# Performance work log

Hardware: AMD Instinct MI355X
Metric: run time of the kernel (lower is better)

## Reference

```python
import jax, jax.numpy as jnp
import numpy as np

B, R, S = 4, 65536, 48  # batch, rays (256x256), depth_resolution


def setup_inputs() -> dict:
    key = jax.random.key(0)
    k1, k2, k3 = jax.random.split(key, 3)
    colors = jax.random.uniform(k1, (B, R, S, 3), dtype=jnp.float32)
    densities = jax.random.normal(k2, (B, R, S, 1), dtype=jnp.float32)
    # stratified depths in [-1, 1], monotone along sample axis (axis=-2)
    depths = jnp.sort(
        jax.random.uniform(k3, (B, R, S, 1), dtype=jnp.float32) * 2.0 - 1.0,
        axis=-2,
    )
    return {"colors": colors, "densities": densities, "depths": depths}


def reference(colors, densities, depths):
    # MipRayMarcher2.run_forward
    deltas = depths[:, :, 1:] - depths[:, :, :-1]                     # [B,R,S-1,1]
    colors_mid = (colors[:, :, :-1] + colors[:, :, 1:]) * 0.5         # [B,R,S-1,3]
    densities_mid = (densities[:, :, :-1] + densities[:, :, 1:]) * 0.5
    depths_mid = (depths[:, :, :-1] + depths[:, :, 1:]) * 0.5

    densities_mid = jax.nn.softplus(densities_mid - 1.0)
    density_delta = densities_mid * deltas
    alpha = 1.0 - jnp.exp(-density_delta)                             # [B,R,S-1,1]

    # exclusive cumulative transmittance along the sample axis
    alpha_shifted = jnp.concatenate(
        [jnp.ones_like(alpha[:, :, :1]), 1.0 - alpha + 1e-10], axis=-2
    )
    weights = alpha * jnp.cumprod(alpha_shifted, axis=-2)[:, :, :-1]  # [B,R,S-1,1]

    composite_rgb = jnp.sum(weights * colors_mid, axis=-2)            # [B,R,3]
    weight_total = jnp.sum(weights, axis=2)                           # [B,R,1]
    composite_depth = jnp.sum(weights * depths_mid, axis=-2) / weight_total
    composite_depth = jnp.nan_to_num(composite_depth, nan=jnp.inf)
    composite_depth = jnp.clip(composite_depth, jnp.min(depths), jnp.max(depths))

    composite_rgb = composite_rgb * 2.0 - 1.0
    return composite_rgb, composite_depth, weights
```

## Files before the change

kernel.cpp:

```cpp
#include <hip/hip_runtime.h>
#include <math.h>


#define S_SAMPLES 48
#define S_INTERVALS 47
#define WR 16
#define PAD 17
#define WAVES 2
#define BT (WAVES * 64)

#define A_OFF 0
#define B_OFF (S_SAMPLES * PAD)
#define WAVE_LDS (2 * S_SAMPLES * PAD)

__global__ __launch_bounds__(BT, 6) void raymarch_kernel(
    const float* __restrict__ colors,
    const float* __restrict__ densities,
    const float* __restrict__ depths,
    float* __restrict__ bmin,
    float* __restrict__ bmax,
    float* __restrict__ out_rgb,
    float* __restrict__ out_depth,
    float* __restrict__ out_w,
    int nRays) {
    __shared__ float smem[WAVES * WAVE_LDS];
    const int wid = threadIdx.x >> 6;
    const int lane = threadIdx.x & 63;
    float* Wb = smem + wid * WAVE_LDS;

    const int waveId = blockIdx.x * WAVES + wid;
    const size_t wray = (size_t)waveId * WR;

    {
        const float4* gdep = (const float4*)(depths + wray * S_SAMPLES);
        const float4* gden = (const float4*)(densities + wray * S_SAMPLES);
#pragma unroll
        for (int k = 0; k < 3; ++k) {
            int fidx = lane + k * 64;
            int g = fidx * 4;
            int ray = g / S_SAMPLES;
            int s = g - ray * S_SAMPLES;
            float4 vd = gdep[fidx];
            float4 vn = gden[fidx];
            Wb[A_OFF + (s + 0) * PAD + ray] = vd.x;
            Wb[A_OFF + (s + 1) * PAD + ray] = vd.y;
            Wb[A_OFF + (s + 2) * PAD + ray] = vd.z;
            Wb[A_OFF + (s + 3) * PAD + ray] = vd.w;
            Wb[B_OFF + (s + 0) * PAD + ray] = vn.x;
            Wb[B_OFF + (s + 1) * PAD + ray] = vn.y;
            Wb[B_OFF + (s + 2) * PAD + ray] = vn.z;
            Wb[B_OFF + (s + 3) * PAD + ray] = vn.w;
        }
    }

    const int r = lane >> 2;
    const int q = lane & 3;

    const float4* gcol4 = (const float4*)(colors + wray * (S_SAMPLES * 3));
    const int f0 = lane, f1 = lane + 64, f2 = lane + 128;
    const int rr0 = f0 / 12, i40 = f0 - rr0 * 12;
    const int rr1 = f1 / 12, i41 = f1 - rr1 * 12;
    const int rr2 = f2 / 12, i42 = f2 - rr2 * 12;
    float4 t0 = gcol4[rr0 * 36 + i40];
    float4 t1 = gcol4[rr1 * 36 + i41];
    float4 t2 = gcol4[rr2 * 36 + i42];

    asm volatile("s_waitcnt lgkmcnt(0)" ::: "memory");

    const int sBase = 12 * q;
    const float LOG2E = 1.4426950408889634f;
    float dPrev = Wb[A_OFF + sBase * PAD + r];
    float nPrev = Wb[B_OFF + sBase * PAD + r];
    const float firstDep = dPrev;

    float T = 1.f, aw = 0.f, ad = 0.f;
    float w0, w1, w2, w3, w4, w5, w6, w7, w8, w9, w10, w11;

#define MSTEP(J, W, HAS)                                               \
    do {                                                               \
        const int row = (HAS) ? (sBase + (J) + 1) : (sBase + 11);      \
        float dN = Wb[A_OFF + row * PAD + r];                          \
        float nN = Wb[B_OFF + row * PAD + r];                          \
        float delta = dN - dPrev;                                      \
        float xs = (0.5f * (nPrev + nN) - 1.f) * LOG2E;                \
        float sp2 = fmaxf(xs, 0.f) + log2f(1.f + exp2f(-fabsf(xs)));   \
        float alpha = (HAS) ? (1.f - exp2f(-delta * sp2)) : 0.f;       \
        W = alpha * T;                                                 \
        T *= (1.f - alpha + 1e-10f);                                   \
        aw += W;                                                       \
        ad = fmaf(W, 0.5f * (dPrev + dN), ad);                         \
        dPrev = dN;                                                    \
        nPrev = nN;                                                    \
    } while (0)

    MSTEP(0, w0, true);
    MSTEP(1, w1, true);
    MSTEP(2, w2, true);
    MSTEP(3, w3, true);
    MSTEP(4, w4, true);
    MSTEP(5, w5, true);
    MSTEP(6, w6, true);
    MSTEP(7, w7, true);
    MSTEP(8, w8, true);
    MSTEP(9, w9, true);
    MSTEP(10, w10, true);
    MSTEP(11, w11, (q < 3));
#undef MSTEP

    float P = T;
    float u1s = __shfl_up(P, 1);
    float pq = (q >= 1) ? P * u1s : P;
    float u2s = __shfl_up(pq, 2);
    float incl = (q >= 2) ? pq * u2s : pq;
    float u3s = __shfl_up(incl, 1);
    float Texc = (q >= 1) ? u3s : 1.f;

    Wb[A_OFF + (sBase + 0) * PAD + r] = w0 * Texc;
    Wb[A_OFF + (sBase + 1) * PAD + r] = w1 * Texc;
    Wb[A_OFF + (sBase + 2) * PAD + r] = w2 * Texc;
    Wb[A_OFF + (sBase + 3) * PAD + r] = w3 * Texc;
    Wb[A_OFF + (sBase + 4) * PAD + r] = w4 * Texc;
    Wb[A_OFF + (sBase + 5) * PAD + r] = w5 * Texc;
    Wb[A_OFF + (sBase + 6) * PAD + r] = w6 * Texc;
    Wb[A_OFF + (sBase + 7) * PAD + r] = w7 * Texc;
    Wb[A_OFF + (sBase + 8) * PAD + r] = w8 * Texc;
    Wb[A_OFF + (sBase + 9) * PAD + r] = w9 * Texc;
    Wb[A_OFF + (sBase + 10) * PAD + r] = w10 * Texc;
    if (q < 3) Wb[A_OFF + (sBase + 11) * PAD + r] = w11 * Texc;

    aw *= Texc;
    ad *= Texc;
#pragma unroll
    for (int off = 1; off <= 2; off <<= 1) {
        aw += __shfl_xor(aw, off);
        ad += __shfl_xor(ad, off);
    }
    if (q == 0) out_depth[wray + r] = ad / aw;

    float mnd = (q == 0) ? firstDep : INFINITY;
    float mxd = (q == 3) ? dPrev : -INFINITY;
#pragma unroll
    for (int off = 32; off; off >>= 1) {
        mnd = fminf(mnd, __shfl_xor(mnd, off));
        mxd = fmaxf(mxd, __shfl_xor(mxd, off));
    }
    if (lane == 0) {
        bmin[waveId] = mnd;
        bmax[waveId] = mxd;
    }

    asm volatile("s_waitcnt lgkmcnt(0)" ::: "memory");

    {
        float* gw = out_w + wray * S_INTERVALS;
#pragma unroll
        for (int k = 0; k < 12; ++k) {
            int g = lane + k * 64;
            if (g < WR * S_INTERVALS) {
                int ray = g / S_INTERVALS;
                int s = g - ray * S_INTERVALS;
                gw[g] = Wb[A_OFF + s * PAD + ray];
            }
        }
    }

    float a0 = 0.f, a1 = 0.f, a2 = 0.f;
#pragma unroll
    for (int c = 0; c < 3; ++c) {
        Wb[B_OFF + (i40 * 4 + 0) * PAD + rr0] = t0.x;
        Wb[B_OFF + (i40 * 4 + 1) * PAD + rr0] = t0.y;
        Wb[B_OFF + (i40 * 4 + 2) * PAD + rr0] = t0.z;
        Wb[B_OFF + (i40 * 4 + 3) * PAD + rr0] = t0.w;
        Wb[B_OFF + (i41 * 4 + 0) * PAD + rr1] = t1.x;
        Wb[B_OFF + (i41 * 4 + 1) * PAD + rr1] = t1.y;
        Wb[B_OFF + (i41 * 4 + 2) * PAD + rr1] = t1.z;
        Wb[B_OFF + (i41 * 4 + 3) * PAD + rr1] = t1.w;
        Wb[B_OFF + (i42 * 4 + 0) * PAD + rr2] = t2.x;
        Wb[B_OFF + (i42 * 4 + 1) * PAD + rr2] = t2.y;
        Wb[B_OFF + (i42 * 4 + 2) * PAD + rr2] = t2.z;
        Wb[B_OFF + (i42 * 4 + 3) * PAD + rr2] = t2.w;
        if (c < 2) {
            float4 n0 = gcol4[rr0 * 36 + (c + 1) * 12 + i40];
            float4 n1 = gcol4[rr1 * 36 + (c + 1) * 12 + i41];
            float4 n2 = gcol4[rr2 * 36 + (c + 1) * 12 + i42];
            asm volatile("s_waitcnt lgkmcnt(0)" ::: "memory");
#pragma unroll
            for (int i = 0; i < 4; ++i) {
                int sl = 4 * q + i;
                int s = c * 16 + sl;
                float wlo = (s >= 1) ? Wb[A_OFF + (s - 1) * PAD + r] : 0.f;
                float whi = (s <= 46) ? Wb[A_OFF + s * PAD + r] : 0.f;
                float v = 0.5f * (wlo + whi);
                a0 = fmaf(v, Wb[B_OFF + (3 * sl + 0) * PAD + r], a0);
                a1 = fmaf(v, Wb[B_OFF + (3 * sl + 1) * PAD + r], a1);
                a2 = fmaf(v, Wb[B_OFF + (3 * sl + 2) * PAD + r], a2);
            }
            t0 = n0;
            t1 = n1;
            t2 = n2;
        } else {
            asm volatile("s_waitcnt lgkmcnt(0)" ::: "memory");
#pragma unroll
            for (int i = 0; i < 4; ++i) {
                int sl = 4 * q + i;
                int s = c * 16 + sl;
                float wlo = (s >= 1) ? Wb[A_OFF + (s - 1) * PAD + r] : 0.f;
                float whi = (s <= 46) ? Wb[A_OFF + s * PAD + r] : 0.f;
                float v = 0.5f * (wlo + whi);
                a0 = fmaf(v, Wb[B_OFF + (3 * sl + 0) * PAD + r], a0);
                a1 = fmaf(v, Wb[B_OFF + (3 * sl + 1) * PAD + r], a1);
                a2 = fmaf(v, Wb[B_OFF + (3 * sl + 2) * PAD + r], a2);
            }
        }
    }

#pragma unroll
    for (int off = 1; off <= 2; off <<= 1) {
        a0 += __shfl_xor(a0, off);
        a1 += __shfl_xor(a1, off);
        a2 += __shfl_xor(a2, off);
    }
    if (q == 0) {
        size_t rb = (wray + r) * 3;
        out_rgb[rb + 0] = fmaf(a0, 2.f, -1.f);
        out_rgb[rb + 1] = fmaf(a1, 2.f, -1.f);
        out_rgb[rb + 2] = fmaf(a2, 2.f, -1.f);
    }
}

__global__ __launch_bounds__(1024) void reduce_minmax_kernel(
    const float* __restrict__ bmin, const float* __restrict__ bmax,
    float* __restrict__ g, int n) {
    float mn = INFINITY, mx = -INFINITY;
    for (int i = threadIdx.x; i < n; i += 1024) {
        mn = fminf(mn, bmin[i]);
        mx = fmaxf(mx, bmax[i]);
    }
#pragma unroll
    for (int off = 32; off; off >>= 1) {
        mn = fminf(mn, __shfl_xor(mn, off));
        mx = fmaxf(mx, __shfl_xor(mx, off));
    }
    __shared__ float smn[16], smx[16];
    const int wid = threadIdx.x >> 6;
    if ((threadIdx.x & 63) == 0) {
        smn[wid] = mn;
        smx[wid] = mx;
    }
    __syncthreads();
    if (threadIdx.x == 0) {
        float m = INFINITY, M = -INFINITY;
#pragma unroll
        for (int i = 0; i < 16; ++i) {
            m = fminf(m, smn[i]);
            M = fmaxf(M, smx[i]);
        }
        g[0] = m;
        g[1] = M;
    }
}

__global__ __launch_bounds__(256) void clamp_depth_kernel(
    float* __restrict__ out_depth, const float* __restrict__ g, int n) {
    int i = blockIdx.x * blockDim.x + threadIdx.x;
    if (i < n) {
        float gmin = g[0];
        float gmax = g[1];
        float d = out_depth[i];
        if (isnan(d)) d = INFINITY;
        d = fminf(fmaxf(d, gmin), gmax);
        out_depth[i] = d;
    }
}

extern "C" void kernel_launch(void* const* d_in, const int* in_sizes, int n_in,
                              void* d_out, int out_size, void* d_ws, size_t ws_size,
                              hipStream_t stream) {
    const float* colors = (const float*)d_in[0];
    const float* densities = (const float*)d_in[1];
    const float* depths = (const float*)d_in[2];

    const int nRays = in_sizes[2] / S_SAMPLES;
    const int nWaves = nRays / WR;
    const int nBlocks = nWaves / WAVES;

    float* out = (float*)d_out;
    float* out_rgb = out;
    float* out_depth = out + (size_t)nRays * 3;
    float* out_w = out + (size_t)nRays * 4;

    float* wsf = (float*)d_ws;
    float* g = wsf;
    float* bmin = wsf + 2;
    float* bmax = wsf + 2 + nWaves;

    raymarch_kernel<<<nBlocks, BT, 0, stream>>>(
        colors, densities, depths, bmin, bmax, out_rgb, out_depth, out_w, nRays);
    reduce_minmax_kernel<<<1, 1024, 0, stream>>>(bmin, bmax, g, nWaves);
    clamp_depth_kernel<<<(nRays + 255) / 256, 256, 0, stream>>>(out_depth, g, nRays);
}
```

Before: 62.81 us.

## Switch LDS staging to ray-major float4 layout and keep weights in registers

Staging in shared memory moves from a sample-major padded layout to a ray-major layout with a 52-float row stride, so global loads, LDS stores and LDS reads all use float4 accesses instead of scalar transposed stores. Each lane reads its 12-sample segment as vector loads. Midpoint weights are built in registers, with a shuffle supplying the neighbour value, instead of being re-read from LDS. The color accumulation is split by lane quarter with branches per chunk, which adds divergence within each 4-lane group. Removing the explicit waitcnt barriers and lowering launch bounds occupancy from 6 to 5 also changes scheduling and register pressure.

New measurement: 63.24 us. About the same (+0.7%).

```diff
diff --git a/kernel.cpp b/kernel.cpp
--- a/kernel.cpp
+++ b/kernel.cpp
@@ -5,15 +5,12 @@
 #define S_SAMPLES 48
 #define S_INTERVALS 47
 #define WR 16
-#define PAD 17
+#define RSTRIDE 52
 #define WAVES 2
 #define BT (WAVES * 64)
-
-#define A_OFF 0
-#define B_OFF (S_SAMPLES * PAD)
-#define WAVE_LDS (2 * S_SAMPLES * PAD)
-
-__global__ __launch_bounds__(BT, 6) void raymarch_kernel(
+#define WAVE_LDS (2 * WR * RSTRIDE)
+
+__global__ __launch_bounds__(BT, 5) void raymarch_kernel(
     const float* __restrict__ colors,
     const float* __restrict__ densities,
     const float* __restrict__ depths,
@@ -23,10 +20,11 @@
     float* __restrict__ out_depth,
     float* __restrict__ out_w,
     int nRays) {
-    __shared__ float smem[WAVES * WAVE_LDS];
+    __shared__ float4 smem4[WAVES * WAVE_LDS / 4];
     const int wid = threadIdx.x >> 6;
     const int lane = threadIdx.x & 63;
-    float* Wb = smem + wid * WAVE_LDS;
+    float* A = (float*)smem4 + wid * WAVE_LDS;
+    float* B = A + WR * RSTRIDE;
 
     const int waveId = blockIdx.x * WAVES + wid;
     const size_t wray = (size_t)waveId * WR;
@@ -37,24 +35,17 @@
 #pragma unroll
         for (int k = 0; k < 3; ++k) {
             int fidx = lane + k * 64;
-            int g = fidx * 4;
-            int ray = g / S_SAMPLES;
-            int s = g - ray * S_SAMPLES;
-            float4 vd = gdep[fidx];
-            float4 vn = gden[fidx];
-            Wb[A_OFF + (s + 0) * PAD + ray] = vd.x;
-            Wb[A_OFF + (s + 1) * PAD + ray] = vd.y;
-            Wb[A_OFF + (s + 2) * PAD + ray] = vd.z;
-            Wb[A_OFF + (s + 3) * PAD + ray] = vd.w;
-            Wb[B_OFF + (s + 0) * PAD + ray] = vn.x;
-            Wb[B_OFF + (s + 1) * PAD + ray] = vn.y;
-            Wb[B_OFF + (s + 2) * PAD + ray] = vn.z;
-            Wb[B_OFF + (s + 3) * PAD + ray] = vn.w;
+            int rr = fidx / 12;
+            int i4 = fidx - rr * 12;
+            *(float4*)&A[rr * RSTRIDE + i4 * 4] = gdep[fidx];
+            *(float4*)&B[rr * RSTRIDE + i4 * 4] = gden[fidx];
         }
     }
 
     const int r = lane >> 2;
     const int q = lane & 3;
+    const int rbase = r * RSTRIDE;
+    const int base = rbase + 12 * q;
 
     const float4* gcol4 = (const float4*)(colors + wray * (S_SAMPLES * 3));
     const int f0 = lane, f1 = lane + 64, f2 = lane + 128;
@@ -65,46 +56,45 @@
     float4 t1 = gcol4[rr1 * 36 + i41];
     float4 t2 = gcol4[rr2 * 36 + i42];
 
-    asm volatile("s_waitcnt lgkmcnt(0)" ::: "memory");
-
-    const int sBase = 12 * q;
+    asm volatile("" ::: "memory");
+
+    const float4 dA = *(const float4*)&A[base + 0];
+    const float4 dB4 = *(const float4*)&A[base + 4];
+    const float4 dC = *(const float4*)&A[base + 8];
+    const float dD = A[base + 12];
+    const float4 nA = *(const float4*)&B[base + 0];
+    const float4 nB4 = *(const float4*)&B[base + 4];
+    const float4 nC = *(const float4*)&B[base + 8];
+    const float nD = B[base + 12];
+
     const float LOG2E = 1.4426950408889634f;
-    float dPrev = Wb[A_OFF + sBase * PAD + r];
-    float nPrev = Wb[B_OFF + sBase * PAD + r];
-    const float firstDep = dPrev;
-
     float T = 1.f, aw = 0.f, ad = 0.f;
     float w0, w1, w2, w3, w4, w5, w6, w7, w8, w9, w10, w11;
 
-#define MSTEP(J, W, HAS)                                               \
+#define MSTEP(dP, dN, nP, nN, W, HAS)                                  \
     do {                                                               \
-        const int row = (HAS) ? (sBase + (J) + 1) : (sBase + 11);      \
-        float dN = Wb[A_OFF + row * PAD + r];                          \
-        float nN = Wb[B_OFF + row * PAD + r];                          \
-        float delta = dN - dPrev;                                      \
-        float xs = (0.5f * (nPrev + nN) - 1.f) * LOG2E;                \
+        float delta = (dN) - (dP);                                     \
+        float xs = (0.5f * ((nP) + (nN)) - 1.f) * LOG2E;               \
         float sp2 = fmaxf(xs, 0.f) + log2f(1.f + exp2f(-fabsf(xs)));   \
         float alpha = (HAS) ? (1.f - exp2f(-delta * sp2)) : 0.f;       \
         W = alpha * T;                                                 \
         T *= (1.f - alpha + 1e-10f);                                   \
         aw += W;                                                       \
-        ad = fmaf(W, 0.5f * (dPrev + dN), ad);                         \
-        dPrev = dN;                                                    \
-        nPrev = nN;                                                    \
+        ad = fmaf(W, 0.5f * ((dP) + (dN)), ad);                        \
     } while (0)
 
-    MSTEP(0, w0, true);
-    MSTEP(1, w1, true);
-    MSTEP(2, w2, true);
-    MSTEP(3, w3, true);
-    MSTEP(4, w4, true);
-    MSTEP(5, w5, true);
-    MSTEP(6, w6, true);
-    MSTEP(7, w7, true);
-    MSTEP(8, w8, true);
-    MSTEP(9, w9, true);
-    MSTEP(10, w10, true);
-    MSTEP(11, w11, (q < 3));
+    MSTEP(dA.x, dA.y, nA.x, nA.y, w0, true);
+    MSTEP(dA.y, dA.z, nA.y, nA.z, w1, true);
+    MSTEP(dA.z, dA.w, nA.z, nA.w, w2, true);
+    MSTEP(dA.w, dB4.x, nA.w, nB4.x, w3, true);
+    MSTEP(dB4.x, dB4.y, nB4.x, nB4.y, w4, true);
+    MSTEP(dB4.y, dB4.z, nB4.y, nB4.z, w5, true);
+    MSTEP(dB4.z, dB4.w, nB4.z, nB4.w, w6, true);
+    MSTEP(dB4.w, dC.x, nB4.w, nC.x, w7, true);
+    MSTEP(dC.x, dC.y, nC.x, nC.y, w8, true);
+    MSTEP(dC.y, dC.z, nC.y, nC.z, w9, true);
+    MSTEP(dC.z, dC.w, nC.z, nC.w, w10, true);
+    MSTEP(dC.w, dD, nC.w, nD, w11, (q < 3));
 #undef MSTEP
 
     float P = T;
@@ -115,18 +105,13 @@
     float u3s = __shfl_up(incl, 1);
     float Texc = (q >= 1) ? u3s : 1.f;
 
-    Wb[A_OFF + (sBase + 0) * PAD + r] = w0 * Texc;
-    Wb[A_OFF + (sBase + 1) * PAD + r] = w1 * Texc;
-    Wb[A_OFF + (sBase + 2) * PAD + r] = w2 * Texc;
-    Wb[A_OFF + (sBase + 3) * PAD + r] = w3 * Texc;
-    Wb[A_OFF + (sBase + 4) * PAD + r] = w4 * Texc;
-    Wb[A_OFF + (sBase + 5) * PAD + r] = w5 * Texc;
-    Wb[A_OFF + (sBase + 6) * PAD + r] = w6 * Texc;
-    Wb[A_OFF + (sBase + 7) * PAD + r] = w7 * Texc;
-    Wb[A_OFF + (sBase + 8) * PAD + r] = w8 * Texc;
-    Wb[A_OFF + (sBase + 9) * PAD + r] = w9 * Texc;
-    Wb[A_OFF + (sBase + 10) * PAD + r] = w10 * Texc;
-    if (q < 3) Wb[A_OFF + (sBase + 11) * PAD + r] = w11 * Texc;
+    float W0 = w0 * Texc, W1 = w1 * Texc, W2 = w2 * Texc, W3 = w3 * Texc;
+    float W4 = w4 * Texc, W5 = w5 * Texc, W6 = w6 * Texc, W7 = w7 * Texc;
+    float W8 = w8 * Texc, W9 = w9 * Texc, W10 = w10 * Texc, W11 = w11 * Texc;
+    asm volatile("" ::: "memory");
+    *(float4*)&A[base + 0] = make_float4(W0, W1, W2, W3);
+    *(float4*)&A[base + 4] = make_float4(W4, W5, W6, W7);
+    *(float4*)&A[base + 8] = make_float4(W8, W9, W10, W11);
 
     aw *= Texc;
     ad *= Texc;
@@ -137,8 +122,8 @@
     }
     if (q == 0) out_depth[wray + r] = ad / aw;
 
-    float mnd = (q == 0) ? firstDep : INFINITY;
-    float mxd = (q == 3) ? dPrev : -INFINITY;
+    float mnd = (q == 0) ? dA.x : INFINITY;
+    float mxd = (q == 3) ? dC.w : -INFINITY;
 #pragma unroll
     for (int off = 32; off; off >>= 1) {
         mnd = fminf(mnd, __shfl_xor(mnd, off));
@@ -149,7 +134,20 @@
         bmax[waveId] = mxd;
     }
 
-    asm volatile("s_waitcnt lgkmcnt(0)" ::: "memory");
+    asm volatile("" : "+v"(t0.x), "+v"(t0.y), "+v"(t0.z), "+v"(t0.w),
+                      "+v"(t1.x), "+v"(t1.y), "+v"(t1.z), "+v"(t1.w),
+                      "+v"(t2.x), "+v"(t2.y), "+v"(t2.z), "+v"(t2.w));
+
+    float Wm1 = __shfl_up(W11, 1);
+    if (q == 0) Wm1 = 0.f;
+    float v0 = 0.5f * (Wm1 + W0), v1 = 0.5f * (W0 + W1);
+    float v2 = 0.5f * (W1 + W2), v3 = 0.5f * (W2 + W3);
+    float v4 = 0.5f * (W3 + W4), v5 = 0.5f * (W4 + W5);
+    float v6 = 0.5f * (W5 + W6), v7 = 0.5f * (W6 + W7);
+    float v8 = 0.5f * (W7 + W8), v9 = 0.5f * (W8 + W9);
+    float v10 = 0.5f * (W9 + W10), v11 = 0.5f * (W10 + W11);
+
+    asm volatile("" ::: "memory");
 
     {
         float* gw = out_w + wray * S_INTERVALS;
@@ -159,60 +157,73 @@
             if (g < WR * S_INTERVALS) {
                 int ray = g / S_INTERVALS;
                 int s = g - ray * S_INTERVALS;
-                gw[g] = Wb[A_OFF + s * PAD + ray];
+                gw[g] = A[ray * RSTRIDE + s];
             }
         }
     }
 
     float a0 = 0.f, a1 = 0.f, a2 = 0.f;
+
+#define ACC4(vA, vB, vC, vD, fa, fb, fc)                                \
+    do {                                                                \
+        a0 = fmaf(vA, (fa).x, a0); a1 = fmaf(vA, (fa).y, a1);           \
+        a2 = fmaf(vA, (fa).z, a2); a0 = fmaf(vB, (fa).w, a0);           \
+        a1 = fmaf(vB, (fb).x, a1); a2 = fmaf(vB, (fb).y, a2);           \
+        a0 = fmaf(vC, (fb).z, a0); a1 = fmaf(vC, (fb).w, a1);           \
+        a2 = fmaf(vC, (fc).x, a2); a0 = fmaf(vD, (fc).y, a0);           \
+        a1 = fmaf(vD, (fc).z, a1); a2 = fmaf(vD, (fc).w, a2);           \
+    } while (0)
+#define LD3(f, loc)                                                     \
+    float4 f##a = *(const float4*)&B[rbase + (loc)];                    \
+    float4 f##b = *(const float4*)&B[rbase + (loc) + 4];                \
+    float4 f##c = *(const float4*)&B[rbase + (loc) + 8];
+
 #pragma unroll
     for (int c = 0; c < 3; ++c) {
-        Wb[B_OFF + (i40 * 4 + 0) * PAD + rr0] = t0.x;
-        Wb[B_OFF + (i40 * 4 + 1) * PAD + rr0] = t0.y;
-        Wb[B_OFF + (i40 * 4 + 2) * PAD + rr0] = t0.z;
-        Wb[B_OFF + (i40 * 4 + 3) * PAD + rr0] = t0.w;
-        Wb[B_OFF + (i41 * 4 + 0) * PAD + rr1] = t1.x;
-        Wb[B_OFF + (i41 * 4 + 1) * PAD + rr1] = t1.y;
-        Wb[B_OFF + (i41 * 4 + 2) * PAD + rr1] = t1.z;
-        Wb[B_OFF + (i41 * 4 + 3) * PAD + rr1] = t1.w;
-        Wb[B_OFF + (i42 * 4 + 0) * PAD + rr2] = t2.x;
-        Wb[B_OFF + (i42 * 4 + 1) * PAD + rr2] = t2.y;
-        Wb[B_OFF + (i42 * 4 + 2) * PAD + rr2] = t2.z;
-        Wb[B_OFF + (i42 * 4 + 3) * PAD + rr2] = t2.w;
+        asm volatile("" ::: "memory");
+        *(float4*)&B[rr0 * RSTRIDE + i40 * 4] = t0;
+        *(float4*)&B[rr1 * RSTRIDE + i41 * 4] = t1;
+        *(float4*)&B[rr2 * RSTRIDE + i42 * 4] = t2;
         if (c < 2) {
-            float4 n0 = gcol4[rr0 * 36 + (c + 1) * 12 + i40];
-            float4 n1 = gcol4[rr1 * 36 + (c + 1) * 12 + i41];
-            float4 n2 = gcol4[rr2 * 36 + (c + 1) * 12 + i42];
-            asm volatile("s_waitcnt lgkmcnt(0)" ::: "memory");
-#pragma unroll
-            for (int i = 0; i < 4; ++i) {
-                int sl = 4 * q + i;
-                int s = c * 16 + sl;
-                float wlo = (s >= 1) ? Wb[A_OFF + (s - 1) * PAD + r] : 0.f;
-                float whi = (s <= 46) ? Wb[A_OFF + s * PAD + r] : 0.f;
-                float v = 0.5f * (wlo + whi);
-                a0 = fmaf(v, Wb[B_OFF + (3 * sl + 0) * PAD + r], a0);
-                a1 = fmaf(v, Wb[B_OFF + (3 * sl + 1) * PAD + r], a1);
-                a2 = fmaf(v, Wb[B_OFF + (3 * sl + 2) * PAD + r], a2);
+            t0 = gcol4[rr0 * 36 + (c + 1) * 12 + i40];
+            t1 = gcol4[rr1 * 36 + (c + 1) * 12 + i41];
+            t2 = gcol4[rr2 * 36 + (c + 1) * 12 + i42];
+        }
+        asm volatile("" ::: "memory");
+        if (c == 0) {
+            if (q == 0) {
+                LD3(x, 0) LD3(y, 12) LD3(z, 24)
+                ACC4(v0, v1, v2, v3, xa, xb, xc);
+                ACC4(v4, v5, v6, v7, ya, yb, yc);
+                ACC4(v8, v9, v10, v11, za, zb, zc);
+            } else if (q == 1) {
+                LD3(x, 36)
+                ACC4(v0, v1, v2, v3, xa, xb, xc);
             }
-            t0 = n0;
-            t1 = n1;
-            t2 = n2;
+        } else if (c == 1) {
+            if (q == 1) {
+                LD3(x, 0) LD3(y, 12)
+                ACC4(v4, v5, v6, v7, xa, xb, xc);
+                ACC4(v8, v9, v10, v11, ya, yb, yc);
+            } else if (q == 2) {
+                LD3(x, 24) LD3(y, 36)
+                ACC4(v0, v1, v2, v3, xa, xb, xc);
+                ACC4(v4, v5, v6, v7, ya, yb, yc);
+            }
         } else {
-            asm volatile("s_waitcnt lgkmcnt(0)" ::: "memory");
-#pragma unroll
-            for (int i = 0; i < 4; ++i) {
-                int sl = 4 * q + i;
-                int s = c * 16 + sl;
-                float wlo = (s >= 1) ? Wb[A_OFF + (s - 1) * PAD + r] : 0.f;
-                float whi = (s <= 46) ? Wb[A_OFF + s * PAD + r] : 0.f;
-                float v = 0.5f * (wlo + whi);
-                a0 = fmaf(v, Wb[B_OFF + (3 * sl + 0) * PAD + r], a0);
-                a1 = fmaf(v, Wb[B_OFF + (3 * sl + 1) * PAD + r], a1);
-                a2 = fmaf(v, Wb[B_OFF + (3 * sl + 2) * PAD + r], a2);
+            if (q == 2) {
+                LD3(x, 0)
+                ACC4(v8, v9, v10, v11, xa, xb, xc);
+            } else if (q == 3) {
+                LD3(x, 12) LD3(y, 24) LD3(z, 36)
+                ACC4(v0, v1, v2, v3, xa, xb, xc);
+                ACC4(v4, v5, v6, v7, ya, yb, yc);
+                ACC4(v8, v9, v10, v11, za, zb, zc);
             }
         }
     }
+#undef LD3
+#undef ACC4
 
 #pragma unroll
     for (int off = 1; off <= 2; off <<= 1) {
```
